# Kernel tuning notes

Measured on AMD Instinct MI355X. Metric: run time of the kernel, lower is better.

## Reference

```python
import jax, jax.numpy as jnp
import numpy as np

B, C, H, W = 2, 1024, 64, 64
R, E, HE, T, K = 16, 4, 512, 3, 2


def setup_inputs() -> dict:
    key = jax.random.key(0)
    ks = jax.random.split(key, 12)
    s = 0.02
    return {
        "x": jax.random.normal(ks[0], (B, C, H, W), jnp.float32),
        "t": jax.random.normal(ks[1], (B, C, H, W), jnp.float32),
        "fc_w": jax.random.normal(ks[2], (C, 2 * C), jnp.float32) * s,
        "ln_g": jnp.ones((C,), jnp.float32),
        "ln_b": jnp.zeros((C,), jnp.float32),
        "f1_w1": jax.random.normal(ks[3], (C // R, C), jnp.float32) * s,
        "f1_b1": jnp.zeros((C // R,), jnp.float32),
        "f1_wa": jax.random.normal(ks[4], (C, C // R), jnp.float32) * s,
        "f1_ba": jnp.zeros((C,), jnp.float32),
        "f1_wb": jax.random.normal(ks[5], (C, C // R), jnp.float32) * s,
        "f1_bb": jnp.zeros((C,), jnp.float32),
        "w_gate": jax.random.normal(ks[6], (T, C, E), jnp.float32) * s,
        "e_w1": jax.random.normal(ks[7], (E, C, HE), jnp.float32) * s,
        "e_b1": jnp.zeros((E, HE), jnp.float32),
        "e_w2": jax.random.normal(ks[8], (E, HE, C), jnp.float32) * s,
        "e_b2": jnp.zeros((E, C), jnp.float32),
        "task_index": 1,
    }


def _cv_squared(v):
    eps = 1e-10
    return jnp.var(v, ddof=1) / (jnp.mean(v) ** 2 + eps)


def reference(x, t, fc_w, ln_g, ln_b, f1_w1, f1_b1, f1_wa, f1_ba, f1_wb, f1_bb,
              w_gate, e_w1, e_b1, e_w2, e_b2, task_index):
    b, c, h, w = x.shape
    n = h * w
    # MultiTaskGeneralFusion: SE-style dual-branch channel gating
    s = jnp.mean(x + t, axis=(2, 3))                        # [B, C]
    hid = jax.nn.relu(s @ f1_w1.T + f1_b1)                  # [B, C/r]
    a = hid @ f1_wa.T + f1_ba                               # [B, C]
    bb = hid @ f1_wb.T + f1_bb                              # [B, C]
    wts = jax.nn.softmax(jnp.stack([a, bb], axis=0), axis=0)  # [2, B, C]
    z = wts[0][:, :, None, None] * x + wts[1][:, :, None, None] * t
    # fused linear -> ReLU -> LayerNorm on concatenated tokens
    x3 = x.reshape(b, c, n).transpose(0, 2, 1)              # [B, N, C]
    t3 = t.reshape(b, c, n).transpose(0, 2, 1)
    y = jnp.concatenate([x3, t3], axis=-1)                  # [B, N, 2C]
    y = jax.nn.relu(jnp.einsum('bnd,cd->bnc', y, fc_w))     # [B, N, C]
    mu = jnp.mean(y, axis=-1, keepdims=True)
    var = jnp.mean((y - mu) ** 2, axis=-1, keepdims=True)
    y = (y - mu) * jax.lax.rsqrt(var + 1e-5) * ln_g + ln_b
    yf = y.reshape(b * n, c)                                # [BN, C]
    # MMoE top-k gating (eval mode: no gating noise)
    logits = yf @ w_gate[task_index]                        # [BN, E]
    top_logits, top_idx = jax.lax.top_k(logits, K)          # [BN, K]
    top_gates = jax.nn.softmax(top_logits, axis=-1)
    gates = jnp.zeros_like(logits).at[jnp.arange(b * n)[:, None], top_idx].set(top_gates)
    # dense expert compute, gated combine
    eh = jax.nn.relu(jnp.einsum('nc,ech->neh', yf, e_w1) + e_b1)   # [BN, E, HE]
    eo = jnp.einsum('neh,eho->neo', eh, e_w2) + e_b2               # [BN, E, C]
    ym = jnp.einsum('ne,neo->no', gates, eo)                        # [BN, C]
    importance = gates.sum(axis=0)
    load = (gates > 0).sum(axis=0).astype(jnp.float32)
    aux_loss = _cv_squared(importance) + _cv_squared(load)
    y4 = ym.reshape(b, n, c).transpose(0, 2, 1).reshape(b, c, h, w) + z
    return (y4, aux_loss)
```

## Files before the change

kernel.cpp:

```cpp
#include <hip/hip_runtime.h>
#include <cstddef>
#include <cstdint>

#define B_   2
#define C_   1024
#define N_   4096
#define M_   8192
#define K2_  2048
#define E_   4
#define HE_  512

typedef float f32x4 __attribute__((ext_vector_type(4)));
typedef short bf16x8 __attribute__((ext_vector_type(8)));
typedef _Float16 f16x8 __attribute__((ext_vector_type(8)));
typedef unsigned short u16x8 __attribute__((ext_vector_type(8)));

#define WAITV(N) asm volatile("s_waitcnt vmcnt(" #N ")" ::: "memory")
#define WAITL0   asm volatile("s_waitcnt lgkmcnt(0)" ::: "memory")

static __device__ __forceinline__ unsigned short f2bf(float f) {
  unsigned int u = __float_as_uint(f);
  u = u + 0x7fffu + ((u >> 16) & 1u);
  return (unsigned short)(u >> 16);
}

static __device__ __forceinline__ void gl_lds16(const void* g, void* l) {
  __builtin_amdgcn_global_load_lds(
      (const __attribute__((address_space(1))) void*)(uintptr_t)g,
      (__attribute__((address_space(3))) void*)(unsigned)(uintptr_t)l,
      16, 0, 0);
}

__global__ __launch_bounds__(256) void k_reduce_s(const float* __restrict__ x,
                                                  const float* __restrict__ t,
                                                  float* __restrict__ s) {
  const int bc = blockIdx.x;
  const float* xp = x + (size_t)bc * N_;
  const float* tp = t + (size_t)bc * N_;
  float acc = 0.f;
  for (int i = threadIdx.x; i < N_ / 4; i += 256) {
    const float4 a = ((const float4*)xp)[i];
    const float4 b = ((const float4*)tp)[i];
    acc += ((a.x + b.x) + (a.y + b.y)) + ((a.z + b.z) + (a.w + b.w));
  }
  #pragma unroll
  for (int o = 32; o; o >>= 1) acc += __shfl_down(acc, o);
  __shared__ float red[4];
  if ((threadIdx.x & 63) == 0) red[threadIdx.x >> 6] = acc;
  __syncthreads();
  if (threadIdx.x == 0)
    s[bc] = (red[0] + red[1] + red[2] + red[3]) * (1.f / (float)N_);
}

__global__ __launch_bounds__(256) void k_se_gate(const float* __restrict__ s,
                                                 const float* __restrict__ w1, const float* __restrict__ b1,
                                                 const float* __restrict__ wa, const float* __restrict__ ba,
                                                 const float* __restrict__ wb, const float* __restrict__ bbv,
                                                 float* __restrict__ wts0) {
  __shared__ float hid[2][64];
  const int t = threadIdx.x;
  if (t < 128) {
    const int b = t >> 6, r = t & 63;
    float acc = b1[r];
    const float* sp = s + b * C_;
    const float* wp = w1 + r * C_;
    for (int c = 0; c < C_; ++c) acc = fmaf(sp[c], wp[c], acc);
    hid[b][r] = fmaxf(acc, 0.f);
  }
  __syncthreads();
  for (int o = t; o < B_ * C_; o += 256) {
    const int b = o >> 10, c = o & 1023;
    float a = ba[c], bb = bbv[c];
    #pragma unroll 8
    for (int r = 0; r < 64; ++r) {
      const float h = hid[b][r];
      a  = fmaf(h, wa[c * 64 + r], a);
      bb = fmaf(h, wb[c * 64 + r], bb);
    }
    wts0[o] = 1.f / (1.f + expf(bb - a));
  }
}

__global__ __launch_bounds__(256) void k_prep_act(const float* __restrict__ x,
                                                  const float* __restrict__ t,
                                                  _Float16* __restrict__ ah,
                                                  _Float16* __restrict__ am) {
  __shared__ float tile[64][65];
  const int c0 = blockIdx.x * 64, n0 = blockIdx.y * 64, b = blockIdx.z;
  const float* xb = x + (size_t)b * (C_ * N_);
  const float* tb = t + (size_t)b * (C_ * N_);
  _Float16* ahb = ah + (size_t)b * (N_ * (size_t)K2_);
  _Float16* amb = am + (size_t)b * (N_ * (size_t)K2_);
  const int tid = threadIdx.x;
  #pragma unroll
  for (int srcsel = 0; srcsel < 2; ++srcsel) {
    const float* src = srcsel ? tb : xb;
    const int koff = srcsel ? C_ : 0;
    if (srcsel) __syncthreads();
    #pragma unroll
    for (int p = 0; p < 4; ++p) {
      const int f = tid + p * 256;
      const int cr = f >> 4, nq = f & 15;
      const float4 v = *(const float4*)(src + (size_t)(c0 + cr) * N_ + n0 + nq * 4);
      tile[cr][nq * 4 + 0] = v.x; tile[cr][nq * 4 + 1] = v.y;
      tile[cr][nq * 4 + 2] = v.z; tile[cr][nq * 4 + 3] = v.w;
    }
    __syncthreads();
    #pragma unroll
    for (int p = 0; p < 2; ++p) {
      const int f = tid + p * 256;
      const int mr = f >> 3, kq = f & 7;
      f16x8 hv, mv;
      #pragma unroll
      for (int u = 0; u < 8; ++u) {
        const float v = tile[kq * 8 + u][mr] * 64.f;
        const _Float16 h = (_Float16)v;
        hv[u] = h;
        mv[u] = (_Float16)(v - (float)h);
      }
      const size_t off = (size_t)(n0 + mr) * K2_ + koff + c0 + kq * 8;
      *(f16x8*)(ahb + off) = hv;
      *(f16x8*)(amb + off) = mv;
    }
  }
}

__global__ __launch_bounds__(256) void k_prep_fcw(const float* __restrict__ w,
                                                  _Float16* __restrict__ wh,
                                                  _Float16* __restrict__ wm) {
  const size_t i = ((size_t)blockIdx.x * 256 + threadIdx.x) * 8;
  const float4 v0 = *(const float4*)(w + i);
  const float4 v1 = *(const float4*)(w + i + 4);
  const float vv[8] = {v0.x, v0.y, v0.z, v0.w, v1.x, v1.y, v1.z, v1.w};
  f16x8 hv, mv;
  #pragma unroll
  for (int u = 0; u < 8; ++u) {
    const float sv = vv[u] * 4096.f;
    const _Float16 h = (_Float16)sv;
    hv[u] = h;
    mv[u] = (_Float16)(sv - (float)h);
  }
  *(f16x8*)(wh + i) = hv;
  *(f16x8*)(wm + i) = mv;
}

__global__ __launch_bounds__(256) void k_prep_tr(const float* __restrict__ src, long long zs, int srs,
                                                 unsigned short* __restrict__ dst, long long zo, int drs) {
  __shared__ float tile[64][65];
  const int c0 = blockIdx.x * 64, r0 = blockIdx.y * 64, z = blockIdx.z;
  const float* s = src + (size_t)z * zs;
  unsigned short* d = dst + (size_t)z * zo;
  const int tid = threadIdx.x;
  #pragma unroll
  for (int p = 0; p < 4; ++p) {
    const int f = tid + p * 256;
    const int rr = f >> 4, cq = f & 15;
    const float4 v = *(const float4*)(s + (size_t)(r0 + rr) * srs + c0 + cq * 4);
    tile[rr][cq * 4 + 0] = v.x; tile[rr][cq * 4 + 1] = v.y;
    tile[rr][cq * 4 + 2] = v.z; tile[rr][cq * 4 + 3] = v.w;
  }
  __syncthreads();
  #pragma unroll
  for (int p = 0; p < 2; ++p) {
    const int f = tid + p * 256;
    const int cr = f >> 3, rq = f & 7;
    u16x8 o;
    #pragma unroll
    for (int u = 0; u < 8; ++u) o[u] = f2bf(tile[rq * 8 + u][cr]);
    *(u16x8*)(d + (size_t)(c0 + cr) * drs + r0 + rq * 8) = o;
  }
}

__global__ __launch_bounds__(256) void k_fc_mfma(const _Float16* __restrict__ Ah,
                                                 const _Float16* __restrict__ Am,
                                                 const _Float16* __restrict__ Bh,
                                                 const _Float16* __restrict__ Bm,
                                                 float* __restrict__ y) {
  __shared__ __align__(16) char lds[2][32768];
  const int tid = threadIdx.x, w = tid >> 6, l = tid & 63;
  const int flat = blockIdx.x + blockIdx.y * 8;
  const int swz = (flat & 7) * 64 + (flat >> 3);
  const int n0 = (swz & 7) * 128, m0 = (swz >> 3) * 128;
  const int wr = w >> 1, wc = w & 1, lg = l >> 4, lr = l & 15;
  f32x4 acc[4][4] = {};
  const int sg = tid >> 7, sr = tid & 127;
  const size_t ga0 = (size_t)(m0 + sr) * K2_ + sg * 8;
  const size_t gb0 = (size_t)(n0 + sr) * K2_ + sg * 8;

  auto STAGE = [&](int buf, int k0) {
    char* b = &lds[buf][0] + w * 1024;
    gl_lds16(Ah + ga0 + k0, b);
    gl_lds16(Ah + ga0 + 16 + k0, b + 4096);
    gl_lds16(Am + ga0 + k0, b + 8192);
    gl_lds16(Am + ga0 + 16 + k0, b + 12288);
    gl_lds16(Bh + gb0 + k0, b + 16384);
    gl_lds16(Bh + gb0 + 16 + k0, b + 20480);
    gl_lds16(Bm + gb0 + k0, b + 24576);
    gl_lds16(Bm + gb0 + 16 + k0, b + 28672);
  };

  STAGE(0, 0);
  STAGE(1, 32);
  for (int it = 0; it < 64; ++it) {
    const int cur = it & 1;
    if (it < 63) { WAITV(8); } else { WAITV(0); }
    __builtin_amdgcn_sched_barrier(0);
    __builtin_amdgcn_s_barrier();
    const char* bb = &lds[cur][0];
    f16x8 a_h[4], a_m[4], b_h[4], b_m[4];
    #pragma unroll
    for (int i = 0; i < 4; ++i) {
      const int off = lg * 2048 + (wr * 64 + i * 16 + lr) * 16;
      a_h[i] = *(const f16x8*)(bb + off);
      a_m[i] = *(const f16x8*)(bb + 8192 + off);
    }
    #pragma unroll
    for (int j = 0; j < 4; ++j) {
      const int off = lg * 2048 + (wc * 64 + j * 16 + lr) * 16;
      b_h[j] = *(const f16x8*)(bb + 16384 + off);
      b_m[j] = *(const f16x8*)(bb + 24576 + off);
    }
    #pragma unroll
    for (int i = 0; i < 4; ++i)
      #pragma unroll
      for (int j = 0; j < 4; ++j)
        acc[i][j] = __builtin_amdgcn_mfma_f32_16x16x32_f16(a_h[i], b_h[j], acc[i][j], 0, 0, 0);
    #pragma unroll
    for (int i = 0; i < 4; ++i)
      #pragma unroll
      for (int j = 0; j < 4; ++j)
        acc[i][j] = __builtin_amdgcn_mfma_f32_16x16x32_f16(a_h[i], b_m[j], acc[i][j], 0, 0, 0);
    #pragma unroll
    for (int i = 0; i < 4; ++i)
      #pragma unroll
      for (int j = 0; j < 4; ++j)
        acc[i][j] = __builtin_amdgcn_mfma_f32_16x16x32_f16(a_m[i], b_h[j], acc[i][j], 0, 0, 0);
    WAITL0;
    __builtin_amdgcn_sched_barrier(0);
    __builtin_amdgcn_s_barrier();
    if (it < 62) STAGE(cur, (it + 2) * 32);
  }
  #pragma unroll
  for (int i = 0; i < 4; ++i) {
    const int mb = m0 + wr * 64 + i * 16 + lg * 4;
    #pragma unroll
    for (int j = 0; j < 4; ++j) {
      const int n = n0 + wc * 64 + j * 16 + lr;
      #pragma unroll
      for (int r = 0; r < 4; ++r)
        y[(size_t)(mb + r) * C_ + n] = fmaxf(acc[i][j][r] * (1.f / 262144.f), 0.f);
    }
  }
}

__global__ __launch_bounds__(256) void k_ln_topk(const float* __restrict__ y,
                                                 const float* __restrict__ lng, const float* __restrict__ lnb,
                                                 const float* __restrict__ wg, const int* __restrict__ taskp,
                                                 unsigned short* __restrict__ yf, float* __restrict__ gates) {
  const int wv = threadIdx.x >> 6, ln = threadIdx.x & 63;
  const int m = blockIdx.x * 4 + wv;
  const float* yr = y + (size_t)m * C_;
  float4 v[4];
  #pragma unroll
  for (int ch = 0; ch < 4; ++ch) v[ch] = *(const float4*)(yr + ch * 256 + ln * 4);
  float sum = 0.f;
  #pragma unroll
  for (int ch = 0; ch < 4; ++ch) sum += (v[ch].x + v[ch].y) + (v[ch].z + v[ch].w);
  #pragma unroll
  for (int o = 32; o; o >>= 1) sum += __shfl_down(sum, o);
  sum = __shfl(sum, 0);
  const float mu = sum * (1.f / 1024.f);
  float q = 0.f;
  #pragma unroll
  for (int ch = 0; ch < 4; ++ch) {
    const float dx = v[ch].x - mu, dy = v[ch].y - mu, dz = v[ch].z - mu, dw = v[ch].w - mu;
    q += (dx * dx + dy * dy) + (dz * dz + dw * dw);
  }
  #pragma unroll
  for (int o = 32; o; o >>= 1) q += __shfl_down(q, o);
  q = __shfl(q, 0);
  const float rstd = rsqrtf(q * (1.f / 1024.f) + 1e-5f);
  const float* wrow = wg + (size_t)(*taskp) * (C_ * E_);
  float l0 = 0.f, l1 = 0.f, l2 = 0.f, l3 = 0.f;
  #pragma unroll
  for (int ch = 0; ch < 4; ++ch) {
    const int c = ch * 256 + ln * 4;
    const float4 gg = *(const float4*)(lng + c);
    const float4 bv = *(const float4*)(lnb + c);
    float f[4];
    f[0] = (v[ch].x - mu) * rstd * gg.x + bv.x;
    f[1] = (v[ch].y - mu) * rstd * gg.y + bv.y;
    f[2] = (v[ch].z - mu) * rstd * gg.z + bv.z;
    f[3] = (v[ch].w - mu) * rstd * gg.w + bv.w;
    uint2 pk;
    pk.x = (unsigned)f2bf(f[0]) | ((unsigned)f2bf(f[1]) << 16);
    pk.y = (unsigned)f2bf(f[2]) | ((unsigned)f2bf(f[3]) << 16);
    *(uint2*)(yf + (size_t)m * C_ + c) = pk;
    #pragma unroll
    for (int i = 0; i < 4; ++i) {
      const float4 we = *(const float4*)(wrow + (size_t)(c + i) * 4);
      l0 = fmaf(f[i], we.x, l0); l1 = fmaf(f[i], we.y, l1);
      l2 = fmaf(f[i], we.z, l2); l3 = fmaf(f[i], we.w, l3);
    }
  }
  #pragma unroll
  for (int o = 32; o; o >>= 1) {
    l0 += __shfl_down(l0, o); l1 += __shfl_down(l1, o);
    l2 += __shfl_down(l2, o); l3 += __shfl_down(l3, o);
  }
  if (ln == 0) {
    const float L[4] = {l0, l1, l2, l3};
    int i1 = 0; float best = L[0];
    #pragma unroll
    for (int e = 1; e < 4; ++e) if (L[e] > best) { best = L[e]; i1 = e; }
    int i2 = -1; float s2 = 0.f;
    #pragma unroll
    for (int e = 0; e < 4; ++e) if (e != i1 && (i2 < 0 || L[e] > s2)) { s2 = L[e]; i2 = e; }
    const float g1 = 1.f / (1.f + expf(s2 - best));
    const float g2 = 1.f - g1;
    float4 gv;
    gv.x = (i1 == 0) ? g1 : ((i2 == 0) ? g2 : 0.f);
    gv.y = (i1 == 1) ? g1 : ((i2 == 1) ? g2 : 0.f);
    gv.z = (i1 == 2) ? g1 : ((i2 == 2) ? g2 : 0.f);
    gv.w = (i1 == 3) ? g1 : ((i2 == 3) ? g2 : 0.f);
    *(float4*)(gates + (size_t)m * 4) = gv;
  }
}

__global__ __launch_bounds__(256) void k_moe1_mfma(const unsigned short* __restrict__ yf,
                                                   const short* __restrict__ Bw,
                                                   const float* __restrict__ b1,
                                                   const float* __restrict__ gates,
                                                   unsigned short* __restrict__ ehg) {
  __shared__ __align__(16) char lds[2][16384];
  const int tid = threadIdx.x, w = tid >> 6, l = tid & 63;
  const int flat = blockIdx.x + blockIdx.y * 16;
  const int swz = (flat & 7) * 128 + (flat >> 3);
  const int n0 = (swz & 15) * 128, m0 = (swz >> 4) * 128;
  const int wr = w >> 1, wc = w & 1, lg = l >> 4, lr = l & 15;
  f32x4 acc[4][4] = {};
  const int sg = tid >> 7, sr = tid & 127;
  const size_t ga0 = (size_t)(m0 + sr) * C_ + sg * 8;
  const size_t gb0 = (size_t)(n0 + sr) * C_ + sg * 8;

  auto STAGE = [&](int buf, int k0) {
    char* b = &lds[buf][0] + w * 1024;
    gl_lds16(yf + ga0 + k0, b);
    gl_lds16(yf + ga0 + 16 + k0, b + 4096);
    gl_lds16(Bw + gb0 + k0, b + 8192);
    gl_lds16(Bw + gb0 + 16 + k0, b + 12288);
  };

  STAGE(0, 0);
  STAGE(1, 32);
  for (int it = 0; it < 32; ++it) {
    const int cur = it & 1;
    if (it < 31) { WAITV(4); } else { WAITV(0); }
    __builtin_amdgcn_sched_barrier(0);
    __builtin_amdgcn_s_barrier();
    const char* bb = &lds[cur][0];
    bf16x8 af[4], bfr[4];
    #pragma unroll
    for (int i = 0; i < 4; ++i)
      af[i] = *(const bf16x8*)(bb + lg * 2048 + (wr * 64 + i * 16 + lr) * 16);
    #pragma unroll
    for (int j = 0; j < 4; ++j)
      bfr[j] = *(const bf16x8*)(bb + 8192 + lg * 2048 + (wc * 64 + j * 16 + lr) * 16);
    #pragma unroll
    for (int i = 0; i < 4; ++i)
      #pragma unroll
      for (int j = 0; j < 4; ++j)
        acc[i][j] = __builtin_amdgcn_mfma_f32_16x16x32_bf16(af[i], bfr[j], acc[i][j], 0, 0, 0);
    WAITL0;
    __builtin_amdgcn_sched_barrier(0);
    __builtin_amdgcn_s_barrier();
    if (it < 30) STAGE(cur, (it + 2) * 32);
  }
  const int e0 = n0 >> 9;
  #pragma unroll
  for (int j = 0; j < 4; ++j) {
    const int n = n0 + wc * 64 + j * 16 + lr;
    const float bias = b1[e0 * HE_ + (n & 511)];
    #pragma unroll
    for (int i = 0; i < 4; ++i) {
      const int mb = m0 + wr * 64 + i * 16 + lg * 4;
      #pragma unroll
      for (int r = 0; r < 4; ++r) {
        const float g = gates[(size_t)(mb + r) * 4 + e0];
        const float v = fmaxf(acc[i][j][r] + bias, 0.f) * g;
        ehg[(size_t)(mb + r) * K2_ + n] = f2bf(v);
      }
    }
  }
}

__global__ __launch_bounds__(256) void k_moe2_mfma(const short* __restrict__ Aeh,
                                                   const short* __restrict__ Bw,
                                                   const float* __restrict__ b2,
                                                   const float* __restrict__ gates,
                                                   float* __restrict__ ym) {
  __shared__ __align__(16) char lds[2][16384];
  const int tid = threadIdx.x, w = tid >> 6, l = tid & 63;
  const int flat = blockIdx.x + blockIdx.y * 8;
  const int swz = (flat & 7) * 64 + (flat >> 3);
  const int n0 = (swz & 7) * 128, m0 = (swz >> 3) * 128;
  const int wr = w >> 1, wc = w & 1, lg = l >> 4, lr = l & 15;
  f32x4 acc[4][4] = {};
  const int sg = tid >> 7, sr = tid & 127;
  const size_t ga0 = (size_t)(m0 + sr) * K2_ + sg * 8;
  const size_t gb0 = (size_t)(n0 + sr) * K2_ + sg * 8;

  auto STAGE = [&](int buf, int k0) {
    char* b = &lds[buf][0] + w * 1024;
    gl_lds16(Aeh + ga0 + k0, b);
    gl_lds16(Aeh + ga0 + 16 + k0, b + 4096);
    gl_lds16(Bw + gb0 + k0, b + 8192);
    gl_lds16(Bw + gb0 + 16 + k0, b + 12288);
  };

  STAGE(0, 0);
  STAGE(1, 32);
  for (int it = 0; it < 64; ++it) {
    const int cur = it & 1;
    if (it < 63) { WAITV(4); } else { WAITV(0); }
    __builtin_amdgcn_sched_barrier(0);
    __builtin_amdgcn_s_barrier();
    const char* bb = &lds[cur][0];
    bf16x8 af[4], bfr[4];
    #pragma unroll
    for (int i = 0; i < 4; ++i)
      af[i] = *(const bf16x8*)(bb + lg * 2048 + (wr * 64 + i * 16 + lr) * 16);
    #pragma unroll
    for (int j = 0; j < 4; ++j)
      bfr[j] = *(const bf16x8*)(bb + 8192 + lg * 2048 + (wc * 64 + j * 16 + lr) * 16);
    #pragma unroll
    for (int i = 0; i < 4; ++i)
      #pragma unroll
      for (int j = 0; j < 4; ++j)
        acc[i][j] = __builtin_amdgcn_mfma_f32_16x16x32_bf16(af[i], bfr[j], acc[i][j], 0, 0, 0);
    WAITL0;
    __builtin_amdgcn_sched_barrier(0);
    __builtin_amdgcn_s_barrier();
    if (it < 62) STAGE(cur, (it + 2) * 32);
  }
  float bb2[4][4];
  #pragma unroll
  for (int j = 0; j < 4; ++j) {
    const int n = n0 + wc * 64 + j * 16 + lr;
    #pragma unroll
    for (int e = 0; e < 4; ++e) bb2[j][e] = b2[e * C_ + n];
  }
  #pragma unroll
  for (int i = 0; i < 4; ++i) {
    const int mb = m0 + wr * 64 + i * 16 + lg * 4;
    #pragma unroll
    for (int r = 0; r < 4; ++r) {
      const float4 g = *(const float4*)(gates + (size_t)(mb + r) * 4);
      #pragma unroll
      for (int j = 0; j < 4; ++j) {
        const int n = n0 + wc * 64 + j * 16 + lr;
        ym[(size_t)(mb + r) * C_ + n] =
            acc[i][j][r] + g.x * bb2[j][0] + g.y * bb2[j][1] + g.z * bb2[j][2] + g.w * bb2[j][3];
      }
    }
  }
}

__global__ __launch_bounds__(256) void k_aux(const float* __restrict__ gates, float* __restrict__ outp) {
  const int t = threadIdx.x;
  float imp[4] = {0, 0, 0, 0}, ld[4] = {0, 0, 0, 0};
  for (int m = t; m < M_; m += 256) {
    const float4 g = *(const float4*)(gates + (size_t)m * 4);
    imp[0] += g.x; imp[1] += g.y; imp[2] += g.z; imp[3] += g.w;
    ld[0] += (g.x > 0.f) ? 1.f : 0.f; ld[1] += (g.y > 0.f) ? 1.f : 0.f;
    ld[2] += (g.z > 0.f) ? 1.f : 0.f; ld[3] += (g.w > 0.f) ? 1.f : 0.f;
  }
  __shared__ float red[8][4];
  const int wv = t >> 6, ln = t & 63;
  #pragma unroll
  for (int e = 0; e < 4; ++e) {
    float a = imp[e], b = ld[e];
    #pragma unroll
    for (int o = 32; o; o >>= 1) { a += __shfl_down(a, o); b += __shfl_down(b, o); }
    if (ln == 0) { red[e][wv] = a; red[4 + e][wv] = b; }
  }
  __syncthreads();
  if (t == 0) {
    float I[4], L[4];
    #pragma unroll
    for (int e = 0; e < 4; ++e) {
      I[e] = red[e][0] + red[e][1] + red[e][2] + red[e][3];
      L[e] = red[4 + e][0] + red[4 + e][1] + red[4 + e][2] + red[4 + e][3];
    }
    const float mi = (I[0] + I[1] + I[2] + I[3]) * 0.25f;
    const float vi = ((I[0] - mi) * (I[0] - mi) + (I[1] - mi) * (I[1] - mi) +
                      (I[2] - mi) * (I[2] - mi) + (I[3] - mi) * (I[3] - mi)) / 3.f;
    const float ml = (L[0] + L[1] + L[2] + L[3]) * 0.25f;
    const float vl = ((L[0] - ml) * (L[0] - ml) + (L[1] - ml) * (L[1] - ml) +
                      (L[2] - ml) * (L[2] - ml) + (L[3] - ml) * (L[3] - ml)) / 3.f;
    *outp = vi / (mi * mi + 1e-10f) + vl / (ml * ml + 1e-10f);
  }
}

__global__ __launch_bounds__(256) void k_final(const float* __restrict__ ym,
                                               const float* __restrict__ x, const float* __restrict__ t,
                                               const float* __restrict__ wts0, float* __restrict__ out) {
  __shared__ float tile[64][65];
  const int c0 = blockIdx.x * 64, n0 = blockIdx.y * 64, b = blockIdx.z;
  const int tid = threadIdx.x;
  #pragma unroll
  for (int p = 0; p < 4; ++p) {
    const int f = tid + p * 256;
    const int row = f >> 4, cq = f & 15;
    const float4 v = *(const float4*)(ym + (size_t)(b * N_ + n0 + row) * C_ + c0 + cq * 4);
    tile[row][cq * 4 + 0] = v.x; tile[row][cq * 4 + 1] = v.y;
    tile[row][cq * 4 + 2] = v.z; tile[row][cq * 4 + 3] = v.w;
  }
  __syncthreads();
  #pragma unroll
  for (int p = 0; p < 4; ++p) {
    const int f = tid + p * 256;
    const int cr = f >> 4, nq = f & 15;
    const int c = c0 + cr;
    const float w0 = wts0[b * C_ + c];
    const float w1 = 1.f - w0;
    const size_t idx = (size_t)(b * C_ + c) * N_ + n0 + nq * 4;
    const float4 xv = *(const float4*)(x + idx);
    const float4 tv = *(const float4*)(t + idx);
    float4 o;
    o.x = tile[nq * 4 + 0][cr] + w0 * xv.x + w1 * tv.x;
    o.y = tile[nq * 4 + 1][cr] + w0 * xv.y + w1 * tv.y;
    o.z = tile[nq * 4 + 2][cr] + w0 * xv.z + w1 * tv.z;
    o.w = tile[nq * 4 + 3][cr] + w0 * xv.w + w1 * tv.w;
    *(float4*)(out + idx) = o;
  }
}

extern "C" void kernel_launch(void* const* d_in, const int* in_sizes, int n_in,
                              void* d_out, int out_size, void* d_ws, size_t ws_size,
                              hipStream_t stream) {
  const float* x     = (const float*)d_in[0];
  const float* t     = (const float*)d_in[1];
  const float* fc_w  = (const float*)d_in[2];
  const float* ln_g  = (const float*)d_in[3];
  const float* ln_b  = (const float*)d_in[4];
  const float* f1_w1 = (const float*)d_in[5];
  const float* f1_b1 = (const float*)d_in[6];
  const float* f1_wa = (const float*)d_in[7];
  const float* f1_ba = (const float*)d_in[8];
  const float* f1_wb = (const float*)d_in[9];
  const float* f1_bb = (const float*)d_in[10];
  const float* w_gate = (const float*)d_in[11];
  const float* e_w1  = (const float*)d_in[12];
  const float* e_b1  = (const float*)d_in[13];
  const float* e_w2  = (const float*)d_in[14];
  const float* e_b2  = (const float*)d_in[15];
  const int*   task  = (const int*)d_in[16];
  float* out = (float*)d_out;

  char* ws = (char*)d_ws;
  float*          y    = (float*)ws;
  _Float16*       ah   = (_Float16*)(ws + 33554432);
  _Float16*       am   = (_Float16*)(ws + 67108864);
  unsigned short* yf   = (unsigned short*)(ws + 33554432);
  unsigned short* ehg  = (unsigned short*)(ws + 50331648);
  _Float16* wh  = (_Float16*)(ws + 100663296);
  _Float16* wm  = (_Float16*)(ws + 104857600);
  short*    w1t = (short*)(ws + 109051904);
  short*    w2t = (short*)(ws + 113246208);
  float* sbuf  = (float*)(ws + 117440512);
  float* wts0  = (float*)(ws + 117448704);
  float* gates = (float*)(ws + 117456896);

  k_reduce_s<<<B_ * C_, 256, 0, stream>>>(x, t, sbuf);
  k_se_gate<<<1, 256, 0, stream>>>(sbuf, f1_w1, f1_b1, f1_wa, f1_ba, f1_wb, f1_bb, wts0);
  k_prep_fcw<<<1024, 256, 0, stream>>>(fc_w, wh, wm);
  k_prep_tr<<<dim3(8, 16, 4), 256, 0, stream>>>(e_w1, 524288LL, 512, (unsigned short*)w1t, 524288LL, 1024);
  k_prep_tr<<<dim3(16, 8, 4), 256, 0, stream>>>(e_w2, 524288LL, 1024, (unsigned short*)w2t, 512LL, 2048);
  k_prep_act<<<dim3(16, 64, 2), 256, 0, stream>>>(x, t, ah, am);
  k_fc_mfma<<<dim3(8, 64), 256, 0, stream>>>(ah, am, wh, wm, y);
  k_ln_topk<<<M_ / 4, 256, 0, stream>>>(y, ln_g, ln_b, w_gate, task, yf, gates);
  k_moe1_mfma<<<dim3(16, 64), 256, 0, stream>>>(yf, w1t, e_b1, gates, ehg);
  k_moe2_mfma<<<dim3(8, 64), 256, 0, stream>>>((const short*)ehg, w2t, e_b2, gates, y);
  k_aux<<<1, 256, 0, stream>>>(gates, out + (size_t)B_ * C_ * N_);
  k_final<<<dim3(C_ / 64, N_ / 64, B_), 256, 0, stream>>>(y, x, t, wts0, out);
}
```

Measured before the change: 424.7 us.

## Rewrite fc GEMM as single-wave 32x32 MFMA tiles with triple-buffered staging

The split-fp16 fc GEMM now runs one 64-thread wave per block on a 128x64 output tile. It uses 32x32x16 MFMA instructions with a 3-stage global-to-LDS pipeline and needs no workgroup barriers, and the grid grows to 16x64 blocks. The MoE GEMMs also raise wave priority around their MFMA bursts with s_setprio. The aim is to drop barrier stalls and use the larger MFMA shape more efficiently. The cost is lower operand reuse per block, since each wave reloads A for only 64 columns, and a different occupancy profile.

Result: slower. 711.3 us (+67.5%).

```diff
diff --git a/kernel.cpp b/kernel.cpp
--- a/kernel.cpp
+++ b/kernel.cpp
@@ -11,12 +11,14 @@
 #define HE_  512
 
 typedef float f32x4 __attribute__((ext_vector_type(4)));
+typedef float f32x16 __attribute__((ext_vector_type(16)));
 typedef short bf16x8 __attribute__((ext_vector_type(8)));
 typedef _Float16 f16x8 __attribute__((ext_vector_type(8)));
 typedef unsigned short u16x8 __attribute__((ext_vector_type(8)));
 
 #define WAITV(N) asm volatile("s_waitcnt vmcnt(" #N ")" ::: "memory")
 #define WAITL0   asm volatile("s_waitcnt lgkmcnt(0)" ::: "memory")
+#define SBAR     __builtin_amdgcn_sched_barrier(0)
 
 static __device__ __forceinline__ unsigned short f2bf(float f) {
   unsigned int u = __float_as_uint(f);
@@ -171,86 +173,85 @@
   }
 }
 
-__global__ __launch_bounds__(256) void k_fc_mfma(const _Float16* __restrict__ Ah,
-                                                 const _Float16* __restrict__ Am,
-                                                 const _Float16* __restrict__ Bh,
-                                                 const _Float16* __restrict__ Bm,
-                                                 float* __restrict__ y) {
-  __shared__ __align__(16) char lds[2][32768];
-  const int tid = threadIdx.x, w = tid >> 6, l = tid & 63;
-  const int flat = blockIdx.x + blockIdx.y * 8;
-  const int swz = (flat & 7) * 64 + (flat >> 3);
-  const int n0 = (swz & 7) * 128, m0 = (swz >> 3) * 128;
-  const int wr = w >> 1, wc = w & 1, lg = l >> 4, lr = l & 15;
-  f32x4 acc[4][4] = {};
-  const int sg = tid >> 7, sr = tid & 127;
-  const size_t ga0 = (size_t)(m0 + sr) * K2_ + sg * 8;
-  const size_t gb0 = (size_t)(n0 + sr) * K2_ + sg * 8;
+__global__ __launch_bounds__(64, 2) void k_fc_mfma(const _Float16* __restrict__ Ah,
+                                                   const _Float16* __restrict__ Am,
+                                                   const _Float16* __restrict__ Bh,
+                                                   const _Float16* __restrict__ Bm,
+                                                   float* __restrict__ y) {
+  __shared__ __align__(16) char lds[3][12288];
+  const int l = threadIdx.x;
+  const int n0 = blockIdx.x * 64, m0 = blockIdx.y * 128;
+  const int kg = l >> 5, lr31 = l & 31;
+  f32x16 acc[4][2] = {};
 
   auto STAGE = [&](int buf, int k0) {
-    char* b = &lds[buf][0] + w * 1024;
-    gl_lds16(Ah + ga0 + k0, b);
-    gl_lds16(Ah + ga0 + 16 + k0, b + 4096);
-    gl_lds16(Am + ga0 + k0, b + 8192);
-    gl_lds16(Am + ga0 + 16 + k0, b + 12288);
-    gl_lds16(Bh + gb0 + k0, b + 16384);
-    gl_lds16(Bh + gb0 + 16 + k0, b + 20480);
-    gl_lds16(Bm + gb0 + k0, b + 24576);
-    gl_lds16(Bm + gb0 + 16 + k0, b + 28672);
+    char* b = &lds[buf][0];
+    #pragma unroll
+    for (int i = 0; i < 4; ++i) {
+      const size_t ga = (size_t)(m0 + (i & 1) * 64 + l) * K2_ + k0 + (i >> 1) * 8;
+      gl_lds16(Ah + ga, b + i * 1024);
+      gl_lds16(Am + ga, b + 4096 + i * 1024);
+    }
+    #pragma unroll
+    for (int i = 0; i < 2; ++i) {
+      const size_t gb = (size_t)(n0 + l) * K2_ + k0 + i * 8;
+      gl_lds16(Bh + gb, b + 8192 + i * 1024);
+      gl_lds16(Bm + gb, b + 10240 + i * 1024);
+    }
   };
 
   STAGE(0, 0);
-  STAGE(1, 32);
-  for (int it = 0; it < 64; ++it) {
-    const int cur = it & 1;
-    if (it < 63) { WAITV(8); } else { WAITV(0); }
-    __builtin_amdgcn_sched_barrier(0);
-    __builtin_amdgcn_s_barrier();
-    const char* bb = &lds[cur][0];
-    f16x8 a_h[4], a_m[4], b_h[4], b_m[4];
+  STAGE(1, 16);
+  STAGE(2, 32);
+  for (int it = 0; it < 128; ++it) {
+    if (it < 126)      { WAITV(24); }
+    else if (it == 126){ WAITV(12); }
+    else               { WAITV(0);  }
+    SBAR;
+    const char* b = &lds[it % 3][0];
+    f16x8 a_h[4], a_m[4], b_h[2], b_m[2];
     #pragma unroll
     for (int i = 0; i < 4; ++i) {
-      const int off = lg * 2048 + (wr * 64 + i * 16 + lr) * 16;
-      a_h[i] = *(const f16x8*)(bb + off);
-      a_m[i] = *(const f16x8*)(bb + 8192 + off);
-    }
-    #pragma unroll
-    for (int j = 0; j < 4; ++j) {
-      const int off = lg * 2048 + (wc * 64 + j * 16 + lr) * 16;
-      b_h[j] = *(const f16x8*)(bb + 16384 + off);
-      b_m[j] = *(const f16x8*)(bb + 24576 + off);
-    }
-    #pragma unroll
-    for (int i = 0; i < 4; ++i)
-      #pragma unroll
-      for (int j = 0; j < 4; ++j)
-        acc[i][j] = __builtin_amdgcn_mfma_f32_16x16x32_f16(a_h[i], b_h[j], acc[i][j], 0, 0, 0);
-    #pragma unroll
-    for (int i = 0; i < 4; ++i)
-      #pragma unroll
-      for (int j = 0; j < 4; ++j)
-        acc[i][j] = __builtin_amdgcn_mfma_f32_16x16x32_f16(a_h[i], b_m[j], acc[i][j], 0, 0, 0);
-    #pragma unroll
-    for (int i = 0; i < 4; ++i)
-      #pragma unroll
-      for (int j = 0; j < 4; ++j)
-        acc[i][j] = __builtin_amdgcn_mfma_f32_16x16x32_f16(a_m[i], b_h[j], acc[i][j], 0, 0, 0);
+      const int off = kg * 2048 + (i * 32 + lr31) * 16;
+      a_h[i] = *(const f16x8*)(b + off);
+      a_m[i] = *(const f16x8*)(b + 4096 + off);
+    }
+    #pragma unroll
+    for (int j = 0; j < 2; ++j) {
+      const int off = kg * 1024 + (j * 32 + lr31) * 16;
+      b_h[j] = *(const f16x8*)(b + 8192 + off);
+      b_m[j] = *(const f16x8*)(b + 10240 + off);
+    }
+    #pragma unroll
+    for (int i = 0; i < 4; ++i)
+      #pragma unroll
+      for (int j = 0; j < 2; ++j)
+        acc[i][j] = __builtin_amdgcn_mfma_f32_32x32x16_f16(a_h[i], b_h[j], acc[i][j], 0, 0, 0);
+    #pragma unroll
+    for (int i = 0; i < 4; ++i)
+      #pragma unroll
+      for (int j = 0; j < 2; ++j)
+        acc[i][j] = __builtin_amdgcn_mfma_f32_32x32x16_f16(a_h[i], b_m[j], acc[i][j], 0, 0, 0);
+    #pragma unroll
+    for (int i = 0; i < 4; ++i)
+      #pragma unroll
+      for (int j = 0; j < 2; ++j)
+        acc[i][j] = __builtin_amdgcn_mfma_f32_32x32x16_f16(a_m[i], b_h[j], acc[i][j], 0, 0, 0);
     WAITL0;
-    __builtin_amdgcn_sched_barrier(0);
-    __builtin_amdgcn_s_barrier();
-    if (it < 62) STAGE(cur, (it + 2) * 32);
-  }
-  #pragma unroll
-  for (int i = 0; i < 4; ++i) {
-    const int mb = m0 + wr * 64 + i * 16 + lg * 4;
-    #pragma unroll
-    for (int j = 0; j < 4; ++j) {
-      const int n = n0 + wc * 64 + j * 16 + lr;
-      #pragma unroll
-      for (int r = 0; r < 4; ++r)
-        y[(size_t)(mb + r) * C_ + n] = fmaxf(acc[i][j][r] * (1.f / 262144.f), 0.f);
-    }
-  }
+    SBAR;
+    if (it < 125) STAGE(it % 3, (it + 3) * 16);
+  }
+  #pragma unroll
+  for (int i = 0; i < 4; ++i)
+    #pragma unroll
+    for (int j = 0; j < 2; ++j) {
+      const int col = n0 + j * 32 + lr31;
+      #pragma unroll
+      for (int r = 0; r < 16; ++r) {
+        const int row = m0 + i * 32 + (r & 3) + ((r >> 2) << 3) + (kg << 2);
+        y[(size_t)row * C_ + col] = fmaxf(acc[i][j][r] * (1.f / 262144.f), 0.f);
+      }
+    }
 }
 
 __global__ __launch_bounds__(256) void k_ln_topk(const float* __restrict__ y,
@@ -356,7 +357,7 @@
   for (int it = 0; it < 32; ++it) {
     const int cur = it & 1;
     if (it < 31) { WAITV(4); } else { WAITV(0); }
-    __builtin_amdgcn_sched_barrier(0);
+    SBAR;
     __builtin_amdgcn_s_barrier();
     const char* bb = &lds[cur][0];
     bf16x8 af[4], bfr[4];
@@ -366,13 +367,16 @@
     #pragma unroll
     for (int j = 0; j < 4; ++j)
       bfr[j] = *(const bf16x8*)(bb + 8192 + lg * 2048 + (wc * 64 + j * 16 + lr) * 16);
+    SBAR;
+    __builtin_amdgcn_s_setprio(1);
     #pragma unroll
     for (int i = 0; i < 4; ++i)
       #pragma unroll
       for (int j = 0; j < 4; ++j)
         acc[i][j] = __builtin_amdgcn_mfma_f32_16x16x32_bf16(af[i], bfr[j], acc[i][j], 0, 0, 0);
+    __builtin_amdgcn_s_setprio(0);
     WAITL0;
-    __builtin_amdgcn_sched_barrier(0);
+    SBAR;
     __builtin_amdgcn_s_barrier();
     if (it < 30) STAGE(cur, (it + 2) * 32);
   }
@@ -423,7 +427,7 @@
   for (int it = 0; it < 64; ++it) {
     const int cur = it & 1;
     if (it < 63) { WAITV(4); } else { WAITV(0); }
-    __builtin_amdgcn_sched_barrier(0);
+    SBAR;
     __builtin_amdgcn_s_barrier();
     const char* bb = &lds[cur][0];
     bf16x8 af[4], bfr[4];
@@ -433,13 +437,16 @@
     #pragma unroll
     for (int j = 0; j < 4; ++j)
       bfr[j] = *(const bf16x8*)(bb + 8192 + lg * 2048 + (wc * 64 + j * 16 + lr) * 16);
+    SBAR;
+    __builtin_amdgcn_s_setprio(1);
     #pragma unroll
     for (int i = 0; i < 4; ++i)
       #pragma unroll
       for (int j = 0; j < 4; ++j)
         acc[i][j] = __builtin_amdgcn_mfma_f32_16x16x32_bf16(af[i], bfr[j], acc[i][j], 0, 0, 0);
+    __builtin_amdgcn_s_setprio(0);
     WAITL0;
-    __builtin_amdgcn_sched_barrier(0);
+    SBAR;
     __builtin_amdgcn_s_barrier();
     if (it < 62) STAGE(cur, (it + 2) * 32);
   }
@@ -578,7 +585,7 @@
   k_prep_tr<<<dim3(8, 16, 4), 256, 0, stream>>>(e_w1, 524288LL, 512, (unsigned short*)w1t, 524288LL, 1024);
   k_prep_tr<<<dim3(16, 8, 4), 256, 0, stream>>>(e_w2, 524288LL, 1024, (unsigned short*)w2t, 512LL, 2048);
   k_prep_act<<<dim3(16, 64, 2), 256, 0, stream>>>(x, t, ah, am);
-  k_fc_mfma<<<dim3(8, 64), 256, 0, stream>>>(ah, am, wh, wm, y);
+  k_fc_mfma<<<dim3(16, 64), 64, 0, stream>>>(ah, am, wh, wm, y);
   k_ln_topk<<<M_ / 4, 256, 0, stream>>>(y, ln_g, ln_b, w_gate, task, yf, gates);
   k_moe1_mfma<<<dim3(16, 64), 256, 0, stream>>>(yf, w1t, e_b1, gates, ehg);
   k_moe2_mfma<<<dim3(8, 64), 256, 0, stream>>>((const short*)ehg, w2t, e_b2, gates, y);
```

## Fuse channel mean reduction into activation prep and raise MFMA wave priority

Applied to the files above, without the earlier changes.

Removes the separate k_reduce_s pass over x and t. Per-tile partial channel sums are now computed inside k_prep_act from the LDS tile it already loads, then combined by a small k_reduce2 kernel before the SE gate. This avoids re-reading 64 MB of input. The two MoE MFMA loops also gain s_setprio(1) around the MFMA block, plus a sched barrier, to favour matrix issue across waves.

After: 416.6 us. About the same (-1.9%).

```diff
diff --git a/kernel.cpp b/kernel.cpp
--- a/kernel.cpp
+++ b/kernel.cpp
@@ -17,6 +17,7 @@
 
 #define WAITV(N) asm volatile("s_waitcnt vmcnt(" #N ")" ::: "memory")
 #define WAITL0   asm volatile("s_waitcnt lgkmcnt(0)" ::: "memory")
+#define SBAR     __builtin_amdgcn_sched_barrier(0)
 
 static __device__ __forceinline__ unsigned short f2bf(float f) {
   unsigned int u = __float_as_uint(f);
@@ -29,27 +30,6 @@
       (const __attribute__((address_space(1))) void*)(uintptr_t)g,
       (__attribute__((address_space(3))) void*)(unsigned)(uintptr_t)l,
       16, 0, 0);
-}
-
-__global__ __launch_bounds__(256) void k_reduce_s(const float* __restrict__ x,
-                                                  const float* __restrict__ t,
-                                                  float* __restrict__ s) {
-  const int bc = blockIdx.x;
-  const float* xp = x + (size_t)bc * N_;
-  const float* tp = t + (size_t)bc * N_;
-  float acc = 0.f;
-  for (int i = threadIdx.x; i < N_ / 4; i += 256) {
-    const float4 a = ((const float4*)xp)[i];
-    const float4 b = ((const float4*)tp)[i];
-    acc += ((a.x + b.x) + (a.y + b.y)) + ((a.z + b.z) + (a.w + b.w));
-  }
-  #pragma unroll
-  for (int o = 32; o; o >>= 1) acc += __shfl_down(acc, o);
-  __shared__ float red[4];
-  if ((threadIdx.x & 63) == 0) red[threadIdx.x >> 6] = acc;
-  __syncthreads();
-  if (threadIdx.x == 0)
-    s[bc] = (red[0] + red[1] + red[2] + red[3]) * (1.f / (float)N_);
 }
 
 __global__ __launch_bounds__(256) void k_se_gate(const float* __restrict__ s,
@@ -84,7 +64,8 @@
 __global__ __launch_bounds__(256) void k_prep_act(const float* __restrict__ x,
                                                   const float* __restrict__ t,
                                                   _Float16* __restrict__ ah,
-                                                  _Float16* __restrict__ am) {
+                                                  _Float16* __restrict__ am,
+                                                  float* __restrict__ spart) {
   __shared__ float tile[64][65];
   const int c0 = blockIdx.x * 64, n0 = blockIdx.y * 64, b = blockIdx.z;
   const float* xb = x + (size_t)b * (C_ * N_);
@@ -92,6 +73,8 @@
   _Float16* ahb = ah + (size_t)b * (N_ * (size_t)K2_);
   _Float16* amb = am + (size_t)b * (N_ * (size_t)K2_);
   const int tid = threadIdx.x;
+  const int prow = tid >> 2, pseg = tid & 3;
+  float psum = 0.f;
   #pragma unroll
   for (int srcsel = 0; srcsel < 2; ++srcsel) {
     const float* src = srcsel ? tb : xb;
@@ -106,6 +89,12 @@
       tile[cr][nq * 4 + 2] = v.z; tile[cr][nq * 4 + 3] = v.w;
     }
     __syncthreads();
+    {
+      float a = 0.f;
+      #pragma unroll
+      for (int u = 0; u < 16; ++u) a += tile[prow][pseg * 16 + u];
+      psum += a;
+    }
     #pragma unroll
     for (int p = 0; p < 2; ++p) {
       const int f = tid + p * 256;
@@ -123,6 +112,20 @@
       *(f16x8*)(amb + off) = mv;
     }
   }
+  psum += __shfl_xor(psum, 1);
+  psum += __shfl_xor(psum, 2);
+  if (pseg == 0)
+    spart[((size_t)(b * C_ + c0 + prow)) * 64 + blockIdx.y] = psum;
+}
+
+__global__ __launch_bounds__(256) void k_reduce2(const float* __restrict__ spart,
+                                                 float* __restrict__ s) {
+  const int idx = blockIdx.x * 256 + threadIdx.x;
+  const float* p = spart + (size_t)idx * 64;
+  float acc = 0.f;
+  #pragma unroll
+  for (int j = 0; j < 64; ++j) acc += p[j];
+  s[idx] = acc * (1.f / (float)N_);
 }
 
 __global__ __launch_bounds__(256) void k_prep_fcw(const float* __restrict__ w,
@@ -204,7 +207,7 @@
   for (int it = 0; it < 64; ++it) {
     const int cur = it & 1;
     if (it < 63) { WAITV(8); } else { WAITV(0); }
-    __builtin_amdgcn_sched_barrier(0);
+    SBAR;
     __builtin_amdgcn_s_barrier();
     const char* bb = &lds[cur][0];
     f16x8 a_h[4], a_m[4], b_h[4], b_m[4];
@@ -236,7 +239,7 @@
       for (int j = 0; j < 4; ++j)
         acc[i][j] = __builtin_amdgcn_mfma_f32_16x16x32_f16(a_m[i], b_h[j], acc[i][j], 0, 0, 0);
     WAITL0;
-    __builtin_amdgcn_sched_barrier(0);
+    SBAR;
     __builtin_amdgcn_s_barrier();
     if (it < 62) STAGE(cur, (it + 2) * 32);
   }
@@ -356,7 +359,7 @@
   for (int it = 0; it < 32; ++it) {
     const int cur = it & 1;
     if (it < 31) { WAITV(4); } else { WAITV(0); }
-    __builtin_amdgcn_sched_barrier(0);
+    SBAR;
     __builtin_amdgcn_s_barrier();
     const char* bb = &lds[cur][0];
     bf16x8 af[4], bfr[4];
@@ -366,13 +369,16 @@
     #pragma unroll
     for (int j = 0; j < 4; ++j)
       bfr[j] = *(const bf16x8*)(bb + 8192 + lg * 2048 + (wc * 64 + j * 16 + lr) * 16);
+    SBAR;
+    __builtin_amdgcn_s_setprio(1);
     #pragma unroll
     for (int i = 0; i < 4; ++i)
       #pragma unroll
       for (int j = 0; j < 4; ++j)
         acc[i][j] = __builtin_amdgcn_mfma_f32_16x16x32_bf16(af[i], bfr[j], acc[i][j], 0, 0, 0);
+    __builtin_amdgcn_s_setprio(0);
     WAITL0;
-    __builtin_amdgcn_sched_barrier(0);
+    SBAR;
     __builtin_amdgcn_s_barrier();
     if (it < 30) STAGE(cur, (it + 2) * 32);
   }
@@ -423,7 +429,7 @@
   for (int it = 0; it < 64; ++it) {
     const int cur = it & 1;
     if (it < 63) { WAITV(4); } else { WAITV(0); }
-    __builtin_amdgcn_sched_barrier(0);
+    SBAR;
     __builtin_amdgcn_s_barrier();
     const char* bb = &lds[cur][0];
     bf16x8 af[4], bfr[4];
@@ -433,13 +439,16 @@
     #pragma unroll
     for (int j = 0; j < 4; ++j)
       bfr[j] = *(const bf16x8*)(bb + 8192 + lg * 2048 + (wc * 64 + j * 16 + lr) * 16);
+    SBAR;
+    __builtin_amdgcn_s_setprio(1);
     #pragma unroll
     for (int i = 0; i < 4; ++i)
       #pragma unroll
       for (int j = 0; j < 4; ++j)
         acc[i][j] = __builtin_amdgcn_mfma_f32_16x16x32_bf16(af[i], bfr[j], acc[i][j], 0, 0, 0);
+    __builtin_amdgcn_s_setprio(0);
     WAITL0;
-    __builtin_amdgcn_sched_barrier(0);
+    SBAR;
     __builtin_amdgcn_s_barrier();
     if (it < 62) STAGE(cur, (it + 2) * 32);
   }
@@ -559,11 +568,12 @@
   float* out = (float*)d_out;
 
   char* ws = (char*)d_ws;
-  float*          y    = (float*)ws;
-  _Float16*       ah   = (_Float16*)(ws + 33554432);
-  _Float16*       am   = (_Float16*)(ws + 67108864);
-  unsigned short* yf   = (unsigned short*)(ws + 33554432);
-  unsigned short* ehg  = (unsigned short*)(ws + 50331648);
+  float*          y     = (float*)ws;
+  float*          spart = (float*)ws;
+  _Float16*       ah    = (_Float16*)(ws + 33554432);
+  _Float16*       am    = (_Float16*)(ws + 67108864);
+  unsigned short* yf    = (unsigned short*)(ws + 33554432);
+  unsigned short* ehg   = (unsigned short*)(ws + 50331648);
   _Float16* wh  = (_Float16*)(ws + 100663296);
   _Float16* wm  = (_Float16*)(ws + 104857600);
   short*    w1t = (short*)(ws + 109051904);
@@ -572,12 +582,12 @@
   float* wts0  = (float*)(ws + 117448704);
   float* gates = (float*)(ws + 117456896);
 
-  k_reduce_s<<<B_ * C_, 256, 0, stream>>>(x, t, sbuf);
-  k_se_gate<<<1, 256, 0, stream>>>(sbuf, f1_w1, f1_b1, f1_wa, f1_ba, f1_wb, f1_bb, wts0);
   k_prep_fcw<<<1024, 256, 0, stream>>>(fc_w, wh, wm);
   k_prep_tr<<<dim3(8, 16, 4), 256, 0, stream>>>(e_w1, 524288LL, 512, (unsigned short*)w1t, 524288LL, 1024);
   k_prep_tr<<<dim3(16, 8, 4), 256, 0, stream>>>(e_w2, 524288LL, 1024, (unsigned short*)w2t, 512LL, 2048);
-  k_prep_act<<<dim3(16, 64, 2), 256, 0, stream>>>(x, t, ah, am);
+  k_prep_act<<<dim3(16, 64, 2), 256, 0, stream>>>(x, t, ah, am, spart);
+  k_reduce2<<<8, 256, 0, stream>>>(spart, sbuf);
+  k_se_gate<<<1, 256, 0, stream>>>(sbuf, f1_w1, f1_b1, f1_wa, f1_ba, f1_wb, f1_bb, wts0);
   k_fc_mfma<<<dim3(8, 64), 256, 0, stream>>>(ah, am, wh, wm, y);
   k_ln_topk<<<M_ / 4, 256, 0, stream>>>(y, ln_g, ln_b, w_gate, task, yf, gates);
   k_moe1_mfma<<<dim3(16, 64), 256, 0, stream>>>(yf, w1t, e_b1, gates, ehg);
```
